# Optimization experiments

Hardware: AMD Instinct MI355X
Metric: run time of the kernel (lower is better)

The kernel has to match this reference:

```python
import jax, jax.numpy as jnp
import numpy as np

N_NODES = 10000
N_EDGES = 160000
DIM = 512
LN_EPS = 1e-5


def setup_inputs() -> dict:
    key = jax.random.key(0)
    ks = jax.random.split(key, 6)
    scale = 1.0 / np.sqrt(DIM)
    h = jax.random.normal(ks[0], (N_NODES, DIM), dtype=jnp.float32)
    edge_index = jax.random.randint(ks[1], (2, N_EDGES), 0, N_NODES, dtype=jnp.int32)
    W_self = jax.random.normal(ks[2], (DIM, DIM), dtype=jnp.float32) * scale
    b_self = jnp.zeros((DIM,), dtype=jnp.float32)
    W_neigh = jax.random.normal(ks[3], (DIM, DIM), dtype=jnp.float32) * scale
    b_neigh = jnp.zeros((DIM,), dtype=jnp.float32)
    ln_gamma = jnp.ones((DIM,), dtype=jnp.float32)
    ln_beta = jnp.zeros((DIM,), dtype=jnp.float32)
    return {"h": h, "edge_index": edge_index, "W_self": W_self, "b_self": b_self,
            "W_neigh": W_neigh, "b_neigh": b_neigh, "ln_gamma": ln_gamma, "ln_beta": ln_beta}


def reference(h, edge_index, W_self, b_self, W_neigh, b_neigh, ln_gamma, ln_beta):
    n = h.shape[0]
    src = edge_index[0]
    dst = edge_index[1]
    # per-edge message: gather dst features, dense linear (torch Linear => x @ W.T + b)
    msg = h[dst] @ W_neigh.T + b_neigh            # [E, dim]
    # scatter-add aggregate into src nodes
    neigh = jax.ops.segment_sum(msg, src, num_segments=n)            # [N, dim]
    deg = jax.ops.segment_sum(jnp.ones(src.shape, h.dtype), src, num_segments=n)
    deg = jnp.maximum(deg, 1.0)
    neigh = neigh / deg[:, None]
    # self transform + relu (dropout is identity in eval)
    out = jax.nn.relu(h @ W_self.T + b_self + neigh)
    # residual LayerNorm
    x = h + out
    mean = jnp.mean(x, axis=-1, keepdims=True)
    var = jnp.mean(jnp.square(x - mean), axis=-1, keepdims=True)
    return (x - mean) * jax.lax.rsqrt(var + LN_EPS) * ln_gamma + ln_beta
```

## Files before the change

kernel.cpp:

```cpp
#include <hip/hip_runtime.h>

#define N_NODES 10000
#define N_PAD   10112
#define N_EDGES 160000
#define DIM     512
#define KDIM    1024
#define CAP     64

#define BM 128
#define BN 128
#define BK 64
#define KITERS (KDIM / BK)

typedef __attribute__((ext_vector_type(8))) short bf16x8;
typedef __attribute__((ext_vector_type(4))) float f32x4;
typedef __attribute__((ext_vector_type(2))) float f32x2;

static __device__ __forceinline__ ushort f2bf(float f) {
    union { float f; unsigned u; } x; x.f = f;
    unsigned u = x.u + 0x7fff + ((x.u >> 16) & 1);
    return (ushort)(u >> 16);
}
static __device__ __forceinline__ float b2f(ushort u) {
    union { unsigned u; float f; } x; x.u = ((unsigned)u) << 16; return x.f;
}

__global__ __launch_bounds__(256) void conv_w(
    const float* __restrict__ Wself, const float* __restrict__ Wneigh,
    ushort* __restrict__ Wc, int* __restrict__ cnt)
{
    int idx = blockIdx.x * 256 + threadIdx.x;
    if (idx < N_NODES) cnt[idx] = 0;
    int c  = idx >> 7;
    int k8 = idx & 127;
    const float* src = (k8 < 64) ? (Wself + (size_t)c * DIM + k8 * 8)
                                 : (Wneigh + (size_t)c * DIM + (k8 - 64) * 8);
    float4 v0 = *(const float4*)src;
    float4 v1 = *(const float4*)(src + 4);
    ushort* dst = Wc + (size_t)c * KDIM + k8 * 8;
    ushort4 o0 = { f2bf(v0.x), f2bf(v0.y), f2bf(v0.z), f2bf(v0.w) };
    ushort4 o1 = { f2bf(v1.x), f2bf(v1.y), f2bf(v1.z), f2bf(v1.w) };
    *(ushort4*)dst = o0;
    *(ushort4*)(dst + 4) = o1;
}

__global__ __launch_bounds__(256) void conv_x(
    const float* __restrict__ h, ushort* __restrict__ X,
    unsigned char* __restrict__ H8,
    const int* __restrict__ eidx, int* __restrict__ cnt, int* __restrict__ col)
{
    int idx = blockIdx.x * 256 + threadIdx.x;
    if (idx < N_EDGES) {
        int s = eidx[idx];
        int d = eidx[N_EDGES + idx];
        int p = atomicAdd(&cnt[s], 1);
        if (p < CAP) col[(s << 6) + p] = d;
    }
    int n  = idx >> 7;
    int k8 = idx & 127;
    if (n >= N_PAD) return;
    ushort* dst = X + (size_t)n * KDIM + k8 * 8;
    if (n >= N_NODES) {
        ushort4 z = {0, 0, 0, 0};
        *(ushort4*)dst = z;
        *(ushort4*)(dst + 4) = z;
        return;
    }
    if (k8 >= 64) return;
    const float* src = h + (size_t)n * DIM + k8 * 8;
    float4 v0 = *(const float4*)src;
    float4 v1 = *(const float4*)(src + 4);
    ushort4 o0 = { f2bf(v0.x), f2bf(v0.y), f2bf(v0.z), f2bf(v0.w) };
    ushort4 o1 = { f2bf(v1.x), f2bf(v1.y), f2bf(v1.z), f2bf(v1.w) };
    *(ushort4*)dst = o0;
    *(ushort4*)(dst + 4) = o1;
    uint2 p8;
    int r0 = 0, r1 = 0;
    r0 = __builtin_amdgcn_cvt_pk_fp8_f32(v0.x, v0.y, r0, false);
    r0 = __builtin_amdgcn_cvt_pk_fp8_f32(v0.z, v0.w, r0, true);
    r1 = __builtin_amdgcn_cvt_pk_fp8_f32(v1.x, v1.y, r1, false);
    r1 = __builtin_amdgcn_cvt_pk_fp8_f32(v1.z, v1.w, r1, true);
    p8.x = (unsigned)r0;
    p8.y = (unsigned)r1;
    *(uint2*)(H8 + (size_t)n * DIM + k8 * 8) = p8;
}

__global__ __launch_bounds__(256) void gather_agg(
    const int* __restrict__ cnt, const int* __restrict__ col,
    const unsigned char* __restrict__ H8,
    ushort* __restrict__ X, float* __restrict__ deg)
{
    int gid  = blockIdx.x * 256 + threadIdx.x;
    int n    = gid >> 6;
    int lane = gid & 63;
    if (n >= N_NODES) return;
    int d  = cnt[n];
    int nk = d < CAP ? d : CAP;

    int myc = (lane < nk) ? col[(n << 6) + lane] : 0;

    f32x2 a01 = {0.f, 0.f}, a23 = {0.f, 0.f}, a45 = {0.f, 0.f}, a67 = {0.f, 0.f};
    int k = 0;
    for (; k + 8 <= nk; k += 8) {
        uint2 v[8];
#pragma unroll
        for (int u = 0; u < 8; ++u) {
            int dst = __shfl(myc, k + u);
            v[u] = *(const uint2*)(H8 + (size_t)dst * DIM + lane * 8);
        }
#pragma unroll
        for (int u = 0; u < 8; ++u) {
            f32x2 d01 = __builtin_amdgcn_cvt_pk_f32_fp8((int)v[u].x, false);
            f32x2 d23 = __builtin_amdgcn_cvt_pk_f32_fp8((int)v[u].x, true);
            f32x2 d45 = __builtin_amdgcn_cvt_pk_f32_fp8((int)v[u].y, false);
            f32x2 d67 = __builtin_amdgcn_cvt_pk_f32_fp8((int)v[u].y, true);
            a01 += d01; a23 += d23; a45 += d45; a67 += d67;
        }
    }
    for (; k < nk; ++k) {
        int dst = __shfl(myc, k);
        uint2 v = *(const uint2*)(H8 + (size_t)dst * DIM + lane * 8);
        a01 += __builtin_amdgcn_cvt_pk_f32_fp8((int)v.x, false);
        a23 += __builtin_amdgcn_cvt_pk_f32_fp8((int)v.x, true);
        a45 += __builtin_amdgcn_cvt_pk_f32_fp8((int)v.y, false);
        a67 += __builtin_amdgcn_cvt_pk_f32_fp8((int)v.y, true);
    }
    float inv = 1.0f / fmaxf((float)d, 1.0f);
    ushort* xr = X + (size_t)n * KDIM + DIM + lane * 8;
    ushort4 o0 = { f2bf(a01[0] * inv), f2bf(a01[1] * inv),
                   f2bf(a23[0] * inv), f2bf(a23[1] * inv) };
    ushort4 o1 = { f2bf(a45[0] * inv), f2bf(a45[1] * inv),
                   f2bf(a67[0] * inv), f2bf(a67[1] * inv) };
    *(ushort4*)xr       = o0;
    *(ushort4*)(xr + 4) = o1;
    if (lane == 0) deg[n] = (float)d;
}

#define MFMA(A, B, C) __builtin_amdgcn_mfma_f32_16x16x32_bf16(A, B, C, 0, 0, 0)

__global__ __launch_bounds__(256) void mfma_gemm(
    const ushort* __restrict__ X, const ushort* __restrict__ Wc,
    const float* __restrict__ deg,
    const float* __restrict__ bself, const float* __restrict__ bneigh,
    ushort* __restrict__ Y)
{
    __shared__ ushort As[2][BM * BK];
    __shared__ ushort Bs[2][BN * BK];

    const int t    = threadIdx.x;
    const int lane = t & 63;
    const int wave = t >> 6;
    const int row0 = blockIdx.y * BM;
    const int col0 = blockIdx.x * BN;
    const int wr   = (wave >> 1) * 64;
    const int wc   = (wave & 1) * 64;
    const int fr   = lane & 15;
    const int fq   = lane >> 4;

#define STAGE(BUF, IT)                                                         \
    {                                                                          \
        const int k0s = (IT) * BK;                                             \
        _Pragma("unroll")                                                      \
        for (int s = 0; s < 4; ++s) {                                          \
            int c = t + s * 256;                                               \
            int row = c >> 3;                                                  \
            int ks = k0s + (((c & 7) ^ (row & 7)) << 3);                       \
            __builtin_amdgcn_global_load_lds(                                  \
                (const __attribute__((address_space(1))) void*)                \
                    (X + (size_t)(row0 + row) * KDIM + ks),                    \
                (__attribute__((address_space(3))) void*)(&As[BUF][c * 8]),    \
                16, 0, 0);                                                     \
        }                                                                      \
        _Pragma("unroll")                                                      \
        for (int s = 0; s < 4; ++s) {                                          \
            int c = t + s * 256;                                               \
            int row = c >> 3;                                                  \
            int ks = k0s + (((c & 7) ^ (row & 7)) << 3);                       \
            __builtin_amdgcn_global_load_lds(                                  \
                (const __attribute__((address_space(1))) void*)                \
                    (Wc + (size_t)(col0 + row) * KDIM + ks),                   \
                (__attribute__((address_space(3))) void*)(&Bs[BUF][c * 8]),    \
                16, 0, 0);                                                     \
        }                                                                      \
    }

    f32x4 acc[4][4];
#pragma unroll
    for (int i = 0; i < 4; ++i)
#pragma unroll
        for (int j = 0; j < 4; ++j) acc[i][j] = (f32x4){0.f, 0.f, 0.f, 0.f};

    STAGE(0, 0);
    __syncthreads();

    int buf = 0;
    for (int it = 0; it < KITERS; ++it) {
        if (it + 1 < KITERS) STAGE(buf ^ 1, it + 1);

        const ushort* as = As[buf];
        const ushort* bs = Bs[buf];
#pragma unroll
        for (int inner = 0; inner < 2; ++inner) {
            const int sw = (((inner * 4 + fq) ^ (fr & 7)) << 3);
            bf16x8 a[4], b[4];
#pragma unroll
            for (int i = 0; i < 4; ++i)
                a[i] = *(const bf16x8*)(as + (wr + i * 16 + fr) * BK + sw);
#pragma unroll
            for (int j = 0; j < 4; ++j)
                b[j] = *(const bf16x8*)(bs + (wc + j * 16 + fr) * BK + sw);
#pragma unroll
            for (int i = 0; i < 4; ++i)
#pragma unroll
                for (int j = 0; j < 4; ++j)
                    acc[i][j] = MFMA(a[i], b[j], acc[i][j]);
        }
        __syncthreads();
        buf ^= 1;
    }

#pragma unroll
    for (int i = 0; i < 4; ++i) {
#pragma unroll
        for (int r = 0; r < 4; ++r) {
            int gr = row0 + wr + i * 16 + fq * 4 + r;
            float hb = (gr < N_NODES && deg[gr] > 0.0f) ? 1.0f : 0.0f;
            ushort* yrow = Y + (size_t)gr * DIM;
#pragma unroll
            for (int j = 0; j < 4; ++j) {
                int gc = col0 + wc + j * 16 + fr;
                float v = fmaxf(acc[i][j][r] + bself[gc] + hb * bneigh[gc], 0.f);
                yrow[gc] = f2bf(v);
            }
        }
    }
}

__global__ __launch_bounds__(256) void ln_kernel(
    const ushort* __restrict__ Y, const float* __restrict__ h,
    const float* __restrict__ g, const float* __restrict__ b,
    float* __restrict__ out)
{
    __shared__ float red[8];
    int n = blockIdx.x;
    int t = threadIdx.x;
    float2 hv = *(const float2*)(h + (size_t)n * DIM + t * 2);
    ushort2 yv = *(const ushort2*)(Y + (size_t)n * DIM + t * 2);
    float v0 = hv.x + b2f(yv.x);
    float v1 = hv.y + b2f(yv.y);
    float s  = v0 + v1;
    float sq = v0 * v0 + v1 * v1;
#pragma unroll
    for (int off = 32; off >= 1; off >>= 1) {
        s  += __shfl_xor(s, off);
        sq += __shfl_xor(sq, off);
    }
    int wave = t >> 6;
    if ((t & 63) == 0) { red[wave] = s; red[4 + wave] = sq; }
    __syncthreads();
    s  = red[0] + red[1] + red[2] + red[3];
    sq = red[4] + red[5] + red[6] + red[7];
    float mean = s * (1.0f / DIM);
    float var  = sq * (1.0f / DIM) - mean * mean;
    float rstd = rsqrtf(var + 1e-5f);
    float2 gv = *(const float2*)(g + t * 2);
    float2 bv = *(const float2*)(b + t * 2);
    float2 o;
    o.x = (v0 - mean) * rstd * gv.x + bv.x;
    o.y = (v1 - mean) * rstd * gv.y + bv.y;
    *(float2*)(out + (size_t)n * DIM + t * 2) = o;
}

extern "C" void kernel_launch(void* const* d_in, const int* in_sizes, int n_in,
                              void* d_out, int out_size, void* d_ws, size_t ws_size,
                              hipStream_t stream)
{
    const float* h      = (const float*)d_in[0];
    const int*   eidx   = (const int*)d_in[1];
    const float* Wself  = (const float*)d_in[2];
    const float* bself  = (const float*)d_in[3];
    const float* Wneigh = (const float*)d_in[4];
    const float* bneigh = (const float*)d_in[5];
    const float* gamma  = (const float*)d_in[6];
    const float* beta   = (const float*)d_in[7];
    float* out = (float*)d_out;

    ushort* X   = (ushort*)d_ws;
    ushort* Wc  = X + (size_t)N_PAD * KDIM;
    ushort* Y   = Wc + (size_t)DIM * KDIM;
    float* deg  = (float*)(Y + (size_t)N_PAD * DIM);
    int* cnt    = (int*)(deg + N_NODES);
    int* col    = cnt + N_NODES;
    unsigned char* H8 = (unsigned char*)(col + (size_t)N_NODES * CAP);

    conv_w<<<(DIM * 128) / 256, 256, 0, stream>>>(Wself, Wneigh, Wc, cnt);
    conv_x<<<(N_PAD * 128) / 256, 256, 0, stream>>>(h, X, H8, eidx, cnt, col);
    gather_agg<<<(N_NODES * 64) / 256, 256, 0, stream>>>(cnt, col, H8, X, deg);

    dim3 gg(DIM / BN, N_PAD / BM);
    mfma_gemm<<<gg, 256, 0, stream>>>(X, Wc, deg, bself, bneigh, Y);

    ln_kernel<<<N_NODES, 256, 0, stream>>>(Y, h, gamma, beta, out);
}
```

Measured before the change: 81.44 us.

## Shrink GEMM row tile to 64 and add XCD-aware workgroup remapping

```diff
diff --git a/kernel.cpp b/kernel.cpp
--- a/kernel.cpp
+++ b/kernel.cpp
@@ -1,16 +1,19 @@
 #include <hip/hip_runtime.h>
 
 #define N_NODES 10000
-#define N_PAD   10112
+#define N_PAD   10048
 #define N_EDGES 160000
 #define DIM     512
 #define KDIM    1024
 #define CAP     64
 
-#define BM 128
+#define BM 64
 #define BN 128
 #define BK 64
 #define KITERS (KDIM / BK)
+#define NWG    ((N_PAD / BM) * (DIM / BN))
+#define SWZ_Q  (NWG / 8)
+#define SWZ_R  (NWG % 8)
 
 typedef __attribute__((ext_vector_type(8))) short bf16x8;
 typedef __attribute__((ext_vector_type(4))) float f32x4;
@@ -110,11 +113,10 @@
         }
 #pragma unroll
         for (int u = 0; u < 8; ++u) {
-            f32x2 d01 = __builtin_amdgcn_cvt_pk_f32_fp8((int)v[u].x, false);
-            f32x2 d23 = __builtin_amdgcn_cvt_pk_f32_fp8((int)v[u].x, true);
-            f32x2 d45 = __builtin_amdgcn_cvt_pk_f32_fp8((int)v[u].y, false);
-            f32x2 d67 = __builtin_amdgcn_cvt_pk_f32_fp8((int)v[u].y, true);
-            a01 += d01; a23 += d23; a45 += d45; a67 += d67;
+            a01 += __builtin_amdgcn_cvt_pk_f32_fp8((int)v[u].x, false);
+            a23 += __builtin_amdgcn_cvt_pk_f32_fp8((int)v[u].x, true);
+            a45 += __builtin_amdgcn_cvt_pk_f32_fp8((int)v[u].y, false);
+            a67 += __builtin_amdgcn_cvt_pk_f32_fp8((int)v[u].y, true);
         }
     }
     for (; k < nk; ++k) {
@@ -147,12 +149,18 @@
     __shared__ ushort As[2][BM * BK];
     __shared__ ushort Bs[2][BN * BK];
 
+    const int orig = blockIdx.x;
+    const int xcd  = orig & 7;
+    const int loc  = orig >> 3;
+    const int wgid = (xcd < SWZ_R ? xcd * (SWZ_Q + 1)
+                                  : SWZ_R * (SWZ_Q + 1) + (xcd - SWZ_R) * SWZ_Q) + loc;
+    const int row0 = (wgid >> 2) * BM;
+    const int col0 = (wgid & 3) * BN;
+
     const int t    = threadIdx.x;
     const int lane = t & 63;
     const int wave = t >> 6;
-    const int row0 = blockIdx.y * BM;
-    const int col0 = blockIdx.x * BN;
-    const int wr   = (wave >> 1) * 64;
+    const int wr   = (wave >> 1) * 32;
     const int wc   = (wave & 1) * 64;
     const int fr   = lane & 15;
     const int fq   = lane >> 4;
@@ -161,7 +169,7 @@
     {                                                                          \
         const int k0s = (IT) * BK;                                             \
         _Pragma("unroll")                                                      \
-        for (int s = 0; s < 4; ++s) {                                          \
+        for (int s = 0; s < 2; ++s) {                                          \
             int c = t + s * 256;                                               \
             int row = c >> 3;                                                  \
             int ks = k0s + (((c & 7) ^ (row & 7)) << 3);                       \
@@ -184,9 +192,9 @@
         }                                                                      \
     }
 
-    f32x4 acc[4][4];
-#pragma unroll
-    for (int i = 0; i < 4; ++i)
+    f32x4 acc[2][4];
+#pragma unroll
+    for (int i = 0; i < 2; ++i)
 #pragma unroll
         for (int j = 0; j < 4; ++j) acc[i][j] = (f32x4){0.f, 0.f, 0.f, 0.f};
 
@@ -202,25 +210,21 @@
 #pragma unroll
         for (int inner = 0; inner < 2; ++inner) {
             const int sw = (((inner * 4 + fq) ^ (fr & 7)) << 3);
-            bf16x8 a[4], b[4];
-#pragma unroll
-            for (int i = 0; i < 4; ++i)
-                a[i] = *(const bf16x8*)(as + (wr + i * 16 + fr) * BK + sw);
-#pragma unroll
-            for (int j = 0; j < 4; ++j)
-                b[j] = *(const bf16x8*)(bs + (wc + j * 16 + fr) * BK + sw);
-#pragma unroll
-            for (int i = 0; i < 4; ++i)
-#pragma unroll
-                for (int j = 0; j < 4; ++j)
-                    acc[i][j] = MFMA(a[i], b[j], acc[i][j]);
+            bf16x8 a0 = *(const bf16x8*)(as + (wr + fr) * BK + sw);
+            bf16x8 a1 = *(const bf16x8*)(as + (wr + 16 + fr) * BK + sw);
+#pragma unroll
+            for (int j = 0; j < 4; ++j) {
+                bf16x8 bv = *(const bf16x8*)(bs + (wc + j * 16 + fr) * BK + sw);
+                acc[0][j] = MFMA(a0, bv, acc[0][j]);
+                acc[1][j] = MFMA(a1, bv, acc[1][j]);
+            }
         }
         __syncthreads();
         buf ^= 1;
     }
 
 #pragma unroll
-    for (int i = 0; i < 4; ++i) {
+    for (int i = 0; i < 2; ++i) {
 #pragma unroll
         for (int r = 0; r < 4; ++r) {
             int gr = row0 + wr + i * 16 + fq * 4 + r;
@@ -297,8 +301,7 @@
     conv_x<<<(N_PAD * 128) / 256, 256, 0, stream>>>(h, X, H8, eidx, cnt, col);
     gather_agg<<<(N_NODES * 64) / 256, 256, 0, stream>>>(cnt, col, H8, X, deg);
 
-    dim3 gg(DIM / BN, N_PAD / BM);
-    mfma_gemm<<<gg, 256, 0, stream>>>(X, Wc, deg, bself, bneigh, Y);
+    mfma_gemm<<<NWG, 256, 0, stream>>>(X, Wc, deg, bself, bneigh, Y);
 
     ln_kernel<<<N_NODES, 256, 0, stream>>>(Y, h, gamma, beta, out);
 }
```

Measured after the change: 71.46 us. 12.3% less time.
